# Kernel tuning notes

Measured on AMD Instinct MI355X. Metric: run time of the kernel, lower is better.

The kernel has to match this reference:

```python
import jax, jax.numpy as jnp
import numpy as np


def setup_inputs() -> dict:
    key = jax.random.key(0)
    x = jax.random.normal(key, (1024, 65536), dtype=jnp.float32)
    return {"x": x, "k": 64}


def reference(x, k):
    # BatchTopK: ReLU, then keep the k*batch largest activations across the
    # ENTIRE flattened batch, zeroing everything else.
    acts = jax.nn.relu(x)
    flat = acts.reshape(-1)                      # [batch * d_sae]
    k_total = k * x.shape[0]
    vals, idx = jax.lax.top_k(flat, k_total)     # global selection
    out = jnp.zeros_like(flat).at[idx].set(vals) # scatter back
    return out.reshape(acts.shape)
```

## Files before the change

### kernel.cpp

```cpp
#include <hip/hip_runtime.h>
#include <stdint.h>


#define HDR_CURSOR 0
#define HDR_FLAG   1
#define HDR_THR    2
#define HDR_ICUT   3
#define HIST_OFF   4096
#define CAND_OFF   16384
#define NBINS      2048u
#define BUCKET_CAP 6144u
#define LDS_STAGE  2048
#define ROWS       1024u
#define SPEC       3.0f
#define BASE_BITS  0x40400000u

typedef float f32x4 __attribute__((ext_vector_type(4)));

__device__ __forceinline__ uint32_t bin_of(uint32_t key) {
  uint32_t off = key - BASE_BITS;
  uint32_t b = off >> 12;
  return b < NBINS ? b : (NBINS - 1u);
}

__global__ void k_init(uint32_t* hdr, uint32_t* ghist, uint32_t force_flag) {
  for (uint32_t i = threadIdx.x; i < 64u + NBINS; i += 256u) {
    if (i < 64u) hdr[i] = 0u;
    else ghist[i - 64u] = 0u;
  }
  if (threadIdx.x == 0u) hdr[HDR_FLAG] = force_flag;
}

__device__ __forceinline__ void push4(float4 a, uint32_t gi,
                                      uint32_t* s_cnt, uint2* s_buf) {
  float m = fmaxf(fmaxf(a.x, a.y), fmaxf(a.z, a.w));
  if (__ballot(m >= SPEC)) {
    if (a.x >= SPEC) { uint32_t p = atomicAdd(s_cnt, 1u); if (p < LDS_STAGE) s_buf[p] = make_uint2(__float_as_uint(a.x), gi); }
    if (a.y >= SPEC) { uint32_t p = atomicAdd(s_cnt, 1u); if (p < LDS_STAGE) s_buf[p] = make_uint2(__float_as_uint(a.y), gi + 1u); }
    if (a.z >= SPEC) { uint32_t p = atomicAdd(s_cnt, 1u); if (p < LDS_STAGE) s_buf[p] = make_uint2(__float_as_uint(a.z), gi + 2u); }
    if (a.w >= SPEC) { uint32_t p = atomicAdd(s_cnt, 1u); if (p < LDS_STAGE) s_buf[p] = make_uint2(__float_as_uint(a.w), gi + 3u); }
  }
}

__global__ __launch_bounds__(256) void k_zero_scan(
    float4* __restrict__ out4, float* __restrict__ out,
    const float4* __restrict__ x4, const float* __restrict__ x,
    uint2* __restrict__ cand, uint32_t* __restrict__ hdr,
    uint32_t* __restrict__ ghist,
    uint32_t cap, uint32_t n4, uint32_t n, uint32_t half) {
  uint32_t g    = blockIdx.x >> 3;
  uint32_t role = g & 1u;
  uint32_t bid  = (g >> 1) * 8u + (blockIdx.x & 7u);
  uint32_t stride = half * 256u;
  uint32_t s4 = stride * 4u;
  uint32_t tail0 = n4 * 4u;

  if (role == 0u) {
    const f32x4 z = {0.f, 0.f, 0.f, 0.f};
    uint32_t i = bid * 256u + threadIdx.x;
    for (; i + 3u * stride < n4; i += s4) {
      __builtin_nontemporal_store(z, (f32x4*)(out4 + i));
      __builtin_nontemporal_store(z, (f32x4*)(out4 + i + stride));
      __builtin_nontemporal_store(z, (f32x4*)(out4 + i + 2u * stride));
      __builtin_nontemporal_store(z, (f32x4*)(out4 + i + 3u * stride));
    }
    for (; i < n4; i += stride)
      __builtin_nontemporal_store(z, (f32x4*)(out4 + i));
    if (bid == 0u && threadIdx.x < (n - tail0))
      out[tail0 + threadIdx.x] = 0.f;
    return;
  }

  __shared__ uint32_t s_cnt;
  __shared__ uint32_t s_base;
  __shared__ uint2 s_buf[LDS_STAGE];
  if (threadIdx.x == 0u) s_cnt = 0u;
  __syncthreads();

  uint32_t i = bid * 256u + threadIdx.x;
  for (; i + 3u * stride < n4; i += s4) {
    float4 a0 = x4[i];
    float4 a1 = x4[i + stride];
    float4 a2 = x4[i + 2u * stride];
    float4 a3 = x4[i + 3u * stride];
    push4(a0, i * 4u, &s_cnt, s_buf);
    push4(a1, (i + stride) * 4u, &s_cnt, s_buf);
    push4(a2, (i + 2u * stride) * 4u, &s_cnt, s_buf);
    push4(a3, (i + 3u * stride) * 4u, &s_cnt, s_buf);
  }
  for (; i < n4; i += stride) {
    float4 a = x4[i];
    push4(a, i * 4u, &s_cnt, s_buf);
  }
  if (bid == 0u && threadIdx.x < (n - tail0)) {
    uint32_t gi = tail0 + threadIdx.x;
    float v = x[gi];
    if (v >= SPEC) { uint32_t p = atomicAdd(&s_cnt, 1u); if (p < LDS_STAGE) s_buf[p] = make_uint2(__float_as_uint(v), gi); }
  }
  __syncthreads();
  uint32_t cnt = s_cnt;
  if (cnt == 0u) return;
  uint32_t wcnt = cnt < (uint32_t)LDS_STAGE ? cnt : (uint32_t)LDS_STAGE;
  if (threadIdx.x == 0u) {
    s_base = atomicAdd(&hdr[HDR_CURSOR], cnt);
    if (cnt > (uint32_t)LDS_STAGE) atomicOr(&hdr[HDR_FLAG], 1u);
  }
  __syncthreads();
  uint32_t base = s_base;
  for (uint32_t j = threadIdx.x; j < wcnt; j += blockDim.x) {
    uint32_t gidx = base + j;
    if (gidx < cap) {
      uint2 c = s_buf[j];
      cand[gidx] = c;
      atomicAdd(&ghist[bin_of(c.x)], 1u);
    }
  }
  if (threadIdx.x == 0u && base + wcnt > cap) atomicOr(&hdr[HDR_FLAG], 1u);
}

__global__ __launch_bounds__(1024) void k_select(
    const uint2* __restrict__ cand, uint32_t* __restrict__ hdr,
    const uint32_t* __restrict__ ghist,
    const int* __restrict__ kptr, uint32_t cap) {
  __shared__ uint32_t h[NBINS];
  __shared__ uint32_t s_sel, s_rank, s_bcnt;
  __shared__ uint2 bkt[BUCKET_CAP];
  uint32_t tid = threadIdx.x;
  uint32_t K = (uint32_t)kptr[0] * ROWS;
  uint32_t M = hdr[HDR_CURSOR];
  if (hdr[HDR_FLAG] != 0u || M > cap || M < K) {
    if (tid == 0u) hdr[HDR_FLAG] = 1u;
    return;
  }
  if (K == 0u) {
    if (tid == 0u) { hdr[HDR_THR] = 0xFFFFFFFFu; hdr[HDR_ICUT] = 0xFFFFFFFFu; }
    return;
  }
  h[tid] = ghist[tid];
  h[tid + 1024u] = ghist[tid + 1024u];
  if (tid == 0u) s_bcnt = 0u;
  __syncthreads();
  if (tid < 64u) {
    uint32_t seg = NBINS >> 6;
    uint32_t base = tid * seg;
    uint32_t lanesum = 0u;
    for (uint32_t j = 0; j < seg; ++j) lanesum += h[base + j];
    uint32_t s = lanesum;
    for (int d = 1; d < 64; d <<= 1) {
      uint32_t v = (uint32_t)__shfl_down((int)s, d, 64);
      if ((int)tid + d < 64) s += v;
    }
    uint32_t above = s - lanesum;
    if (above < K && above + lanesum >= K) {
      uint32_t r = K - above;
      uint32_t cum = 0u;
      for (int j = (int)seg - 1; j >= 0; --j) {
        uint32_t c = h[base + (uint32_t)j];
        if (cum + c >= r) { s_sel = base + (uint32_t)j; s_rank = r - cum; break; }
        cum += c;
      }
    }
  }
  __syncthreads();
  uint32_t bsel = s_sel;
  uint32_t r = s_rank;
  uint32_t E = h[bsel];
  if (bsel == NBINS - 1u || E > BUCKET_CAP) {
    if (tid == 0u) hdr[HDR_FLAG] = 1u;
    return;
  }
  const uint4* __restrict__ cand4 = (const uint4*)cand;
  uint32_t M2 = M >> 1;
  uint32_t j = tid;
  for (; j + 3072u < M2; j += 4096u) {
    uint4 c0 = cand4[j];
    uint4 c1 = cand4[j + 1024u];
    uint4 c2 = cand4[j + 2048u];
    uint4 c3 = cand4[j + 3072u];
    if (bin_of(c0.x) == bsel) { uint32_t p = atomicAdd(&s_bcnt, 1u); if (p < BUCKET_CAP) bkt[p] = make_uint2(c0.x, c0.y); }
    if (bin_of(c0.z) == bsel) { uint32_t p = atomicAdd(&s_bcnt, 1u); if (p < BUCKET_CAP) bkt[p] = make_uint2(c0.z, c0.w); }
    if (bin_of(c1.x) == bsel) { uint32_t p = atomicAdd(&s_bcnt, 1u); if (p < BUCKET_CAP) bkt[p] = make_uint2(c1.x, c1.y); }
    if (bin_of(c1.z) == bsel) { uint32_t p = atomicAdd(&s_bcnt, 1u); if (p < BUCKET_CAP) bkt[p] = make_uint2(c1.z, c1.w); }
    if (bin_of(c2.x) == bsel) { uint32_t p = atomicAdd(&s_bcnt, 1u); if (p < BUCKET_CAP) bkt[p] = make_uint2(c2.x, c2.y); }
    if (bin_of(c2.z) == bsel) { uint32_t p = atomicAdd(&s_bcnt, 1u); if (p < BUCKET_CAP) bkt[p] = make_uint2(c2.z, c2.w); }
    if (bin_of(c3.x) == bsel) { uint32_t p = atomicAdd(&s_bcnt, 1u); if (p < BUCKET_CAP) bkt[p] = make_uint2(c3.x, c3.y); }
    if (bin_of(c3.z) == bsel) { uint32_t p = atomicAdd(&s_bcnt, 1u); if (p < BUCKET_CAP) bkt[p] = make_uint2(c3.z, c3.w); }
  }
  for (; j < M2; j += 1024u) {
    uint4 c = cand4[j];
    if (bin_of(c.x) == bsel) { uint32_t p = atomicAdd(&s_bcnt, 1u); if (p < BUCKET_CAP) bkt[p] = make_uint2(c.x, c.y); }
    if (bin_of(c.z) == bsel) { uint32_t p = atomicAdd(&s_bcnt, 1u); if (p < BUCKET_CAP) bkt[p] = make_uint2(c.z, c.w); }
  }
  if (tid == 0u && (M & 1u)) {
    uint2 c = cand[M - 1u];
    if (bin_of(c.x) == bsel) { uint32_t p = atomicAdd(&s_bcnt, 1u); if (p < BUCKET_CAP) bkt[p] = c; }
  }
  __syncthreads();
  for (uint32_t e = tid; e < E; e += 1024u) {
    uint2 me = bkt[e];
    uint32_t rank = 0u;
    for (uint32_t jj = 0; jj < E; ++jj) {
      uint2 o = bkt[jj];
      rank += (o.x > me.x || (o.x == me.x && o.y < me.y)) ? 1u : 0u;
    }
    if (rank == r - 1u) { hdr[HDR_THR] = me.x; hdr[HDR_ICUT] = me.y; }
  }
}

__global__ __launch_bounds__(256) void k_scatter(
    const uint2* __restrict__ cand, const uint32_t* __restrict__ hdr,
    float* __restrict__ out, uint32_t cap) {
  if (hdr[HDR_FLAG] != 0u) return;
  uint32_t M = hdr[HDR_CURSOR]; if (M > cap) M = cap;
  uint32_t thr = hdr[HDR_THR], icut = hdr[HDR_ICUT];
  uint32_t stride = gridDim.x * blockDim.x;
  for (uint32_t i = blockIdx.x * blockDim.x + threadIdx.x; i < M; i += stride) {
    uint2 c = cand[i];
    if (c.x > thr || (c.x == thr && c.y <= icut)) out[c.y] = __uint_as_float(c.x);
  }
}

__global__ __launch_bounds__(1024) void k_fallback(
    const float* __restrict__ x, float* __restrict__ out,
    const int* __restrict__ kptr, const uint32_t* __restrict__ hdr, uint32_t n) {
  if (hdr[HDR_FLAG] == 0u) return;
  __shared__ uint32_t hist[2048];
  __shared__ uint32_t s_sel, s_rank, s_found, s_eqcnt, s_icut;
  __shared__ uint32_t eq_idx[4096];
  uint32_t tid = threadIdx.x;
  uint32_t K = (uint32_t)kptr[0] * ROWS;
  uint32_t prefix = 0u;
  uint32_t R = K;
  bool zero_thr = (K == 0u);
  for (int lvl = 0; lvl < 3 && !zero_thr; ++lvl) {
    uint32_t shift = (lvl == 0) ? 21u : (lvl == 1 ? 10u : 0u);
    uint32_t nb = (lvl == 2) ? 1024u : 2048u;
    for (uint32_t b = tid; b < nb; b += 1024u) hist[b] = 0u;
    __syncthreads();
    for (uint32_t i = tid; i < n; i += 1024u) {
      float v = x[i];
      uint32_t key = (v > 0.f) ? __float_as_uint(v) : 0u;
      bool valid = (key != 0u);
      if (lvl == 1) valid = valid && ((key >> 21) == prefix);
      if (lvl == 2) valid = valid && ((key >> 10) == prefix);
      if (valid) atomicAdd(&hist[(key >> shift) & (nb - 1u)], 1u);
    }
    __syncthreads();
    if (tid == 0u) {
      uint32_t cum = 0u, sel = 0u, rr = R, found = 0u;
      for (int b = (int)nb - 1; b >= 0; --b) {
        uint32_t c = hist[b];
        if (cum + c >= R) { sel = (uint32_t)b; rr = R - cum; found = 1u; break; }
        cum += c;
      }
      s_sel = sel; s_rank = rr; s_found = found;
    }
    __syncthreads();
    if (s_found == 0u) {
      zero_thr = true;
    } else {
      uint32_t sel = s_sel;
      R = s_rank;
      if (lvl == 0) prefix = sel;
      else if (lvl == 1) prefix = (prefix << 11) | sel;
      else prefix = (prefix << 10) | sel;
    }
    __syncthreads();
  }
  uint32_t thr_key = zero_thr ? 0u : prefix;
  uint32_t icut = 0xFFFFFFFFu;
  if (!zero_thr) {
    uint32_t E = hist[thr_key & 1023u];
    uint32_t T = R;
    if (T < E) {
      if (tid == 0u) { s_eqcnt = 0u; s_icut = 0xFFFFFFFFu; }
      __syncthreads();
      for (uint32_t i = tid; i < n; i += 1024u) {
        float v = x[i];
        if (v > 0.f && __float_as_uint(v) == thr_key) {
          uint32_t p = atomicAdd(&s_eqcnt, 1u);
          if (p < 4096u) eq_idx[p] = i;
        }
      }
      __syncthreads();
      uint32_t ec = s_eqcnt < 4096u ? s_eqcnt : 4096u;
      for (uint32_t e = tid; e < ec; e += 1024u) {
        uint32_t me = eq_idx[e];
        uint32_t rank = 0u;
        for (uint32_t j = 0; j < ec; ++j) rank += (eq_idx[j] < me) ? 1u : 0u;
        if (rank == T - 1u) s_icut = me;
      }
      __syncthreads();
      icut = s_icut;
    }
  }
  for (uint32_t i = tid; i < n; i += 1024u) {
    float v = x[i];
    uint32_t key = (v > 0.f) ? __float_as_uint(v) : 0u;
    bool keep = (key > thr_key) || (key != 0u && key == thr_key && i <= icut);
    out[i] = keep ? v : 0.f;
  }
}

extern "C" void kernel_launch(void* const* d_in, const int* in_sizes, int n_in,
                              void* d_out, int out_size, void* d_ws, size_t ws_size,
                              hipStream_t stream) {
  const float* x = (const float*)d_in[0];
  const int* kptr = (const int*)d_in[1];
  float* out = (float*)d_out;
  uint32_t n = (uint32_t)in_sizes[0];
  uint32_t n4 = n >> 2;

  uint32_t* hdr = (uint32_t*)d_ws;
  uint32_t* ghist = (uint32_t*)((char*)d_ws + HIST_OFF);
  uint2* cand = (uint2*)((char*)d_ws + CAND_OFF);
  uint32_t cap = (ws_size > (size_t)CAND_OFF) ? (uint32_t)((ws_size - CAND_OFF) / 8) : 0u;
  uint32_t force = (cap < 131072u) ? 1u : 0u;

  const uint32_t HALF = 2048u;
  k_init<<<1, 256, 0, stream>>>(hdr, ghist, force);
  k_zero_scan<<<2u * HALF, 256, 0, stream>>>((float4*)out, out, (const float4*)x, x,
                                             cand, hdr, ghist, cap, n4, n, HALF);
  k_select<<<1, 1024, 0, stream>>>(cand, hdr, ghist, kptr, cap);
  k_fallback<<<1, 1024, 0, stream>>>(x, out, kptr, hdr, n);
  k_scatter<<<512, 256, 0, stream>>>(cand, hdr, out, cap);
}
```

Baseline: 529.2 us.

## Split fused zero/scan kernel into separate scan and zero kernels

Replaces the combined kernel, which interleaved zero-fill blocks and scan blocks, with two separate launches: a scan kernel that reads the input and collects candidates, and a zero kernel that clears the output. The scan loop now issues 8 float4 loads per iteration before any ballot checks, to keep more memory loads in flight. The per-block LDS staging buffer shrinks from 2048 to 1024 entries, which lowers shared memory use per block. In exchange the read and write traffic no longer overlap within a single launch, and the smaller buffer makes overflow into the fallback path more likely.

```diff
diff --git a/kernel.cpp b/kernel.cpp
--- a/kernel.cpp
+++ b/kernel.cpp
@@ -10,7 +10,7 @@
 #define CAND_OFF   16384
 #define NBINS      2048u
 #define BUCKET_CAP 6144u
-#define LDS_STAGE  2048
+#define SCAN_STAGE 1024
 #define ROWS       1024u
 #define SPEC       3.0f
 #define BASE_BITS  0x40400000u
@@ -23,6 +23,10 @@
   return b < NBINS ? b : (NBINS - 1u);
 }
 
+__device__ __forceinline__ float max4(float4 a) {
+  return fmaxf(fmaxf(a.x, a.y), fmaxf(a.z, a.w));
+}
+
 __global__ void k_init(uint32_t* hdr, uint32_t* ghist, uint32_t force_flag) {
   for (uint32_t i = threadIdx.x; i < 64u + NBINS; i += 256u) {
     if (i < 64u) hdr[i] = 0u;
@@ -33,77 +37,62 @@
 
 __device__ __forceinline__ void push4(float4 a, uint32_t gi,
                                       uint32_t* s_cnt, uint2* s_buf) {
-  float m = fmaxf(fmaxf(a.x, a.y), fmaxf(a.z, a.w));
-  if (__ballot(m >= SPEC)) {
-    if (a.x >= SPEC) { uint32_t p = atomicAdd(s_cnt, 1u); if (p < LDS_STAGE) s_buf[p] = make_uint2(__float_as_uint(a.x), gi); }
-    if (a.y >= SPEC) { uint32_t p = atomicAdd(s_cnt, 1u); if (p < LDS_STAGE) s_buf[p] = make_uint2(__float_as_uint(a.y), gi + 1u); }
-    if (a.z >= SPEC) { uint32_t p = atomicAdd(s_cnt, 1u); if (p < LDS_STAGE) s_buf[p] = make_uint2(__float_as_uint(a.z), gi + 2u); }
-    if (a.w >= SPEC) { uint32_t p = atomicAdd(s_cnt, 1u); if (p < LDS_STAGE) s_buf[p] = make_uint2(__float_as_uint(a.w), gi + 3u); }
-  }
-}
-
-__global__ __launch_bounds__(256) void k_zero_scan(
-    float4* __restrict__ out4, float* __restrict__ out,
+  if (a.x >= SPEC) { uint32_t p = atomicAdd(s_cnt, 1u); if (p < SCAN_STAGE) s_buf[p] = make_uint2(__float_as_uint(a.x), gi); }
+  if (a.y >= SPEC) { uint32_t p = atomicAdd(s_cnt, 1u); if (p < SCAN_STAGE) s_buf[p] = make_uint2(__float_as_uint(a.y), gi + 1u); }
+  if (a.z >= SPEC) { uint32_t p = atomicAdd(s_cnt, 1u); if (p < SCAN_STAGE) s_buf[p] = make_uint2(__float_as_uint(a.z), gi + 2u); }
+  if (a.w >= SPEC) { uint32_t p = atomicAdd(s_cnt, 1u); if (p < SCAN_STAGE) s_buf[p] = make_uint2(__float_as_uint(a.w), gi + 3u); }
+}
+
+__global__ __launch_bounds__(256) void k_scan(
     const float4* __restrict__ x4, const float* __restrict__ x,
     uint2* __restrict__ cand, uint32_t* __restrict__ hdr,
     uint32_t* __restrict__ ghist,
-    uint32_t cap, uint32_t n4, uint32_t n, uint32_t half) {
-  uint32_t g    = blockIdx.x >> 3;
-  uint32_t role = g & 1u;
-  uint32_t bid  = (g >> 1) * 8u + (blockIdx.x & 7u);
-  uint32_t stride = half * 256u;
-  uint32_t s4 = stride * 4u;
-  uint32_t tail0 = n4 * 4u;
-
-  if (role == 0u) {
-    const f32x4 z = {0.f, 0.f, 0.f, 0.f};
-    uint32_t i = bid * 256u + threadIdx.x;
-    for (; i + 3u * stride < n4; i += s4) {
-      __builtin_nontemporal_store(z, (f32x4*)(out4 + i));
-      __builtin_nontemporal_store(z, (f32x4*)(out4 + i + stride));
-      __builtin_nontemporal_store(z, (f32x4*)(out4 + i + 2u * stride));
-      __builtin_nontemporal_store(z, (f32x4*)(out4 + i + 3u * stride));
-    }
-    for (; i < n4; i += stride)
-      __builtin_nontemporal_store(z, (f32x4*)(out4 + i));
-    if (bid == 0u && threadIdx.x < (n - tail0))
-      out[tail0 + threadIdx.x] = 0.f;
-    return;
-  }
-
+    uint32_t cap, uint32_t n4, uint32_t n) {
   __shared__ uint32_t s_cnt;
   __shared__ uint32_t s_base;
-  __shared__ uint2 s_buf[LDS_STAGE];
+  __shared__ uint2 s_buf[SCAN_STAGE];
   if (threadIdx.x == 0u) s_cnt = 0u;
   __syncthreads();
 
-  uint32_t i = bid * 256u + threadIdx.x;
-  for (; i + 3u * stride < n4; i += s4) {
+  uint32_t stride = gridDim.x * blockDim.x;
+  uint32_t i = blockIdx.x * blockDim.x + threadIdx.x;
+  for (; i + 7u * stride < n4; i += 8u * stride) {
     float4 a0 = x4[i];
     float4 a1 = x4[i + stride];
     float4 a2 = x4[i + 2u * stride];
     float4 a3 = x4[i + 3u * stride];
-    push4(a0, i * 4u, &s_cnt, s_buf);
-    push4(a1, (i + stride) * 4u, &s_cnt, s_buf);
-    push4(a2, (i + 2u * stride) * 4u, &s_cnt, s_buf);
-    push4(a3, (i + 3u * stride) * 4u, &s_cnt, s_buf);
+    float4 a4 = x4[i + 4u * stride];
+    float4 a5 = x4[i + 5u * stride];
+    float4 a6 = x4[i + 6u * stride];
+    float4 a7 = x4[i + 7u * stride];
+    float m0 = max4(a0), m1 = max4(a1), m2 = max4(a2), m3 = max4(a3);
+    float m4 = max4(a4), m5 = max4(a5), m6 = max4(a6), m7 = max4(a7);
+    if (__ballot(m0 >= SPEC)) push4(a0, (i) * 4u, &s_cnt, s_buf);
+    if (__ballot(m1 >= SPEC)) push4(a1, (i + stride) * 4u, &s_cnt, s_buf);
+    if (__ballot(m2 >= SPEC)) push4(a2, (i + 2u * stride) * 4u, &s_cnt, s_buf);
+    if (__ballot(m3 >= SPEC)) push4(a3, (i + 3u * stride) * 4u, &s_cnt, s_buf);
+    if (__ballot(m4 >= SPEC)) push4(a4, (i + 4u * stride) * 4u, &s_cnt, s_buf);
+    if (__ballot(m5 >= SPEC)) push4(a5, (i + 5u * stride) * 4u, &s_cnt, s_buf);
+    if (__ballot(m6 >= SPEC)) push4(a6, (i + 6u * stride) * 4u, &s_cnt, s_buf);
+    if (__ballot(m7 >= SPEC)) push4(a7, (i + 7u * stride) * 4u, &s_cnt, s_buf);
   }
   for (; i < n4; i += stride) {
     float4 a = x4[i];
-    push4(a, i * 4u, &s_cnt, s_buf);
-  }
-  if (bid == 0u && threadIdx.x < (n - tail0)) {
+    if (__ballot(max4(a) >= SPEC)) push4(a, i * 4u, &s_cnt, s_buf);
+  }
+  uint32_t tail0 = n4 * 4u;
+  if (blockIdx.x == 0u && threadIdx.x < (n - tail0)) {
     uint32_t gi = tail0 + threadIdx.x;
     float v = x[gi];
-    if (v >= SPEC) { uint32_t p = atomicAdd(&s_cnt, 1u); if (p < LDS_STAGE) s_buf[p] = make_uint2(__float_as_uint(v), gi); }
+    if (v >= SPEC) { uint32_t p = atomicAdd(&s_cnt, 1u); if (p < SCAN_STAGE) s_buf[p] = make_uint2(__float_as_uint(v), gi); }
   }
   __syncthreads();
   uint32_t cnt = s_cnt;
   if (cnt == 0u) return;
-  uint32_t wcnt = cnt < (uint32_t)LDS_STAGE ? cnt : (uint32_t)LDS_STAGE;
+  uint32_t wcnt = cnt < (uint32_t)SCAN_STAGE ? cnt : (uint32_t)SCAN_STAGE;
   if (threadIdx.x == 0u) {
     s_base = atomicAdd(&hdr[HDR_CURSOR], cnt);
-    if (cnt > (uint32_t)LDS_STAGE) atomicOr(&hdr[HDR_FLAG], 1u);
+    if (cnt > (uint32_t)SCAN_STAGE) atomicOr(&hdr[HDR_FLAG], 1u);
   }
   __syncthreads();
   uint32_t base = s_base;
@@ -116,6 +105,20 @@
     }
   }
   if (threadIdx.x == 0u && base + wcnt > cap) atomicOr(&hdr[HDR_FLAG], 1u);
+}
+
+__global__ __launch_bounds__(256) void k_zero(
+    float4* __restrict__ out4, float* __restrict__ out,
+    uint32_t n4, uint32_t n) {
+  const f32x4 z = {0.f, 0.f, 0.f, 0.f};
+  uint32_t stride = gridDim.x * blockDim.x;
+  uint32_t i = blockIdx.x * blockDim.x + threadIdx.x;
+#pragma unroll 4
+  for (; i < n4; i += stride)
+    __builtin_nontemporal_store(z, (f32x4*)(out4 + i));
+  uint32_t tail0 = n4 * 4u;
+  if (blockIdx.x == 0u && threadIdx.x < (n - tail0))
+    out[tail0 + threadIdx.x] = 0.f;
 }
 
 __global__ __launch_bounds__(1024) void k_select(
@@ -317,10 +320,9 @@
   uint32_t cap = (ws_size > (size_t)CAND_OFF) ? (uint32_t)((ws_size - CAND_OFF) / 8) : 0u;
   uint32_t force = (cap < 131072u) ? 1u : 0u;
 
-  const uint32_t HALF = 2048u;
   k_init<<<1, 256, 0, stream>>>(hdr, ghist, force);
-  k_zero_scan<<<2u * HALF, 256, 0, stream>>>((float4*)out, out, (const float4*)x, x,
-                                             cand, hdr, ghist, cap, n4, n, HALF);
+  k_scan<<<2048, 256, 0, stream>>>((const float4*)x, x, cand, hdr, ghist, cap, n4, n);
+  k_zero<<<2048, 256, 0, stream>>>((float4*)out, out, n4, n);
   k_select<<<1, 1024, 0, stream>>>(cand, hdr, ghist, kptr, cap);
   k_fallback<<<1, 1024, 0, stream>>>(x, out, kptr, hdr, n);
   k_scatter<<<512, 256, 0, stream>>>(cand, hdr, out, cap);
```

New measurement: 508.6 us. 1.04x faster.
